# Optimization experiments

Measured on AMD Instinct MI355X. Metric: run time of the kernel, lower is better.

The kernel has to match this reference:

```python
import jax, jax.numpy as jnp
import numpy as np
from jax import lax

SIGMA = 0.03
ALPHA = 1.0
MASK_VALUE = -1e-8
SAMPLE_NUM = 131072  # static stand-in for the dynamic edge-pixel count


def _sobel_edges(images):
    # images: [n,3,h,w]; torch code uses only channel 0 when c==3
    kx = jnp.array([[-1., 0., 1.], [-2., 0., 2.], [-1., 0., 1.]], dtype=images.dtype).reshape(1, 1, 3, 3)
    ky = jnp.array([[1., 2., 1.], [0., 0., 0.], [-1., -2., -1.]], dtype=images.dtype).reshape(1, 1, 3, 3)
    x = images[:, :1]
    dn = ('NCHW', 'OIHW', 'NCHW')
    gx = lax.conv_general_dilated(x, kx, (1, 1), 'VALID', dimension_numbers=dn)
    gy = lax.conv_general_dilated(x, ky, (1, 1), 'VALID', dimension_numbers=dn)
    edges = jnp.sqrt(gx * gx + gy * gy)
    thetas = jnp.arctan2(gy, gx)
    pad = ((0, 0), (0, 0), (1, 1), (1, 1))
    return jnp.pad(edges, pad), jnp.pad(thetas, pad)


def _per_image_loss(inp, tgt, msk, edge, theta, ra, rd, rp, h, w):
    # all flat vectors of length P = h*w; ra:[S], rd:[4,S], rp:[2S]
    # --- edge-guided sampling ---
    emax = edge.max()
    emask = edge >= 0.1 * emax
    minlen = jnp.maximum(emask.sum(), 1)
    edge_idx = jnp.argsort(jnp.logical_not(emask), stable=True)  # edge pixels first
    anchor_pix = edge_idx[ra % minlen]
    theta_a = theta[anchor_pix]
    row_a = anchor_pix // w
    col_a = anchor_pix % w
    sign = jnp.array([-1., -1., 1., 1.], dtype=inp.dtype)[:, None]
    dist = (rd.astype(inp.dtype) + 2.0) * sign  # magnitudes in [2,31)
    col4 = jnp.clip(col_a[None, :] + jnp.round(dist * jnp.cos(theta_a)[None, :]).astype(jnp.int32), 0, w - 1)
    row4 = jnp.clip(row_a[None, :] + jnp.round(dist * jnp.sin(theta_a)[None, :]).astype(jnp.int32), 0, h - 1)
    pix = row4 * w + col4  # sub2ind, [4,S]
    A = jnp.concatenate([pix[0], pix[1], pix[2]])  # [3S]
    B = jnp.concatenate([pix[1], pix[2], pix[3]])
    # --- random sampling among valid (targets > threshold) pixels ---
    vmask = tgt > MASK_VALUE
    nvalid = jnp.maximum(vmask.sum(), 1)
    vidx = jnp.argsort(jnp.logical_not(vmask), stable=True)
    sh = rp % nvalid
    rA = vidx[sh[0::2]]
    rB = vidx[sh[1::2]]
    Ai = jnp.concatenate([A, rA])  # [4S]
    Bi = jnp.concatenate([B, rB])
    iA, iB = inp[Ai], inp[Bi]
    tA, tB = tgt[Ai], tgt[Bi]
    mA, mB = msk[Ai], msk[Bi]
    # --- ranking loss ---
    ratio = (tA + 1e-6) / (tB + 1e-6)
    hi = 1.0 + SIGMA
    lo = 1.0 / hi
    mask_eq = (ratio < hi) & (ratio > lo)
    labels = jnp.where(ratio >= hi, 1.0, 0.0) + jnp.where(ratio <= lo, -1.0, 0.0)
    cm = mA * mB
    equal_loss = (iA - iB) ** 2 * mask_eq.astype(inp.dtype) * cm
    unequal_loss = jnp.log1p(jnp.exp((iB - iA) * labels)) * (~mask_eq).astype(inp.dtype) * cm
    return ALPHA * equal_loss.mean() + unequal_loss.mean()


def reference(inputs, targets, images, rand_anchor, rand_dist, rand_perm):
    n, c, h, w = targets.shape
    masks = (targets > MASK_VALUE).astype(targets.dtype)
    edges, thetas = _sobel_edges(images)
    P = h * w
    flat = lambda x: x.reshape(n, P)
    per_img = lambda i, t, m, e, th, ra, rd, rp: _per_image_loss(i, t, m, e, th, ra, rd, rp, h, w)
    losses = jax.vmap(per_img)(flat(inputs), flat(targets), flat(masks), flat(edges), flat(thetas),
                               rand_anchor, rand_dist, rand_perm)
    return (losses.sum() / n).astype(jnp.float32)


def setup_inputs() -> dict:
    key = jax.random.key(0)
    k1, k2, k3, k4, k5, k6 = jax.random.split(key, 6)
    n, h, w = 4, 768, 1024
    P = h * w
    S = SAMPLE_NUM
    return {
        'inputs': jax.random.normal(k1, (n, 1, h, w), dtype=jnp.float32),
        'targets': jax.random.uniform(k2, (n, 1, h, w), dtype=jnp.float32),
        'images': jax.random.uniform(k3, (n, 3, h, w), dtype=jnp.float32),
        'rand_anchor': jax.random.randint(k4, (n, S), 0, P, dtype=jnp.int32),
        'rand_dist': jax.random.randint(k5, (n, 4, S), 0, 29, dtype=jnp.int32),
        'rand_perm': jax.random.randint(k6, (n, 2 * S), 0, P, dtype=jnp.int32),
    }
```

## Files before the change

kernel.cpp:

```cpp
#include <hip/hip_runtime.h>
#include <math.h>

#define W 1024
#define H 768
#define PIX (W*H)
#define NIMG 4
#define SNUM 131072
#define BPI 3072
#define NB (NIMG*BPI)
#define MASKV (-1e-8f)

__device__ __forceinline__ void sobel_g(const float* __restrict__ img, int y, int x,
                                        float& gx, float& gy) {
    const float* r0 = img + (y - 1) * W + x;
    const float* r1 = r0 + W;
    const float* r2 = r1 + W;
    float a00 = r0[-1], a01 = r0[0], a02 = r0[1];
    float a10 = r1[-1],              a12 = r1[1];
    float a20 = r2[-1], a21 = r2[0], a22 = r2[1];
    gx = (a02 - a00) + 2.f * (a12 - a10) + (a22 - a20);
    gy = (a00 - a20) + 2.f * (a01 - a21) + (a02 - a22);
}

__global__ void prep_kernel(const float* __restrict__ inputs,
                            const float* __restrict__ targets,
                            const float* __restrict__ images,
                            float2* __restrict__ pairIT,
                            unsigned long long* __restrict__ vBits,
                            float* __restrict__ blockmax,
                            int* __restrict__ blkV) {
    int b = blockIdx.x, t = threadIdx.x;
    int i = b / BPI, bLoc = b - i * BPI;
    int gp = bLoc * 256 + t;
    int y = gp >> 10, x = gp & (W - 1);
    const float* img = images + (size_t)i * 3 * PIX;
    float e = 0.f;
    if (y >= 1 && y <= H - 2 && x >= 1 && x <= W - 2) {
        float gx, gy;
        sobel_g(img, y, x, gx, gy);
        e = sqrtf(gx * gx + gy * gy);
    }
    size_t off = (size_t)i * PIX + gp;
    float inv = inputs[off], tgv = targets[off];
    pairIT[off] = make_float2(inv, tgv);
    unsigned long long m = __ballot(tgv > MASKV);
    __shared__ float sm[256];
    __shared__ int sc[4];
    if ((t & 63) == 0) { vBits[off >> 6] = m; sc[t >> 6] = __popcll(m); }
    sm[t] = e;
    __syncthreads();
    for (int o = 128; o > 0; o >>= 1) {
        if (t < o) sm[t] = fmaxf(sm[t], sm[t + o]);
        __syncthreads();
    }
    if (t == 0) { blockmax[b] = sm[0]; blkV[b] = sc[0] + sc[1] + sc[2] + sc[3]; }
}

__global__ void compact_kernel(const float* __restrict__ images,
                               const float* __restrict__ blockmax,
                               const int* __restrict__ blkV,
                               const unsigned long long* __restrict__ vBits,
                               float2* __restrict__ anchorSeg,
                               int* __restrict__ compVSeg,
                               int* __restrict__ cntE,
                               int* __restrict__ SVg,
                               int* __restrict__ vtotG) {
    int b = blockIdx.x, t = threadIdx.x;
    int i = b / BPI, bLoc = b - i * BPI;

    __shared__ float sf[256];
    const float* bm = blockmax + i * BPI;
    float mx = 0.f;
#pragma unroll
    for (int k = 0; k < 12; k++) mx = fmaxf(mx, bm[t + k * 256]);
    sf[t] = mx;
    __syncthreads();
    for (int o = 128; o > 0; o >>= 1) {
        if (t < o) sf[t] = fmaxf(sf[t], sf[t + o]);
        __syncthreads();
    }
    float thr = 0.1f * sf[0];

    int gp = bLoc * 256 + t;
    int y = gp >> 10, x = gp & (W - 1);
    const float* img = images + (size_t)i * 3 * PIX;
    float e = 0.f, gx = 0.f, gy = 0.f;
    bool inner = (y >= 1 && y <= H - 2 && x >= 1 && x <= W - 2);
    if (inner) { sobel_g(img, y, x, gx, gy); e = sqrtf(gx * gx + gy * gy); }
    bool isE = (e >= thr);

    int lane = t & 63, w = t >> 6;
    unsigned long long mE = __ballot(isE);
    size_t woff = ((size_t)i * PIX + bLoc * 256) >> 6;
    unsigned long long mV = vBits[woff + w];
    __shared__ int sW[4], sWV[4];
    if (lane == 0) { sW[w] = __popcll(mE); sWV[w] = __popcll(mV); }
    __syncthreads();
    int baseE = 0, baseV = 0;
    for (int k = 0; k < w; k++) { baseE += sW[k]; baseV += sWV[k]; }
    if (t == 0) cntE[b] = sW[0] + sW[1] + sW[2] + sW[3];
    unsigned long long lm = (1ull << lane) - 1ull;
    if (isE) {
        float th = inner ? atan2f(gy, gx) : 0.f;
        int rank = baseE + __popcll(mE & lm);
        anchorSeg[(size_t)i * PIX + bLoc * 256 + rank] = make_float2(__int_as_float(gp), th);
    }
    if ((mV >> lane) & 1) {
        int rank = baseV + __popcll(mV & lm);
        compVSeg[(size_t)i * PIX + bLoc * 256 + rank] = gp;
    }

    if (bLoc == 0) {
        __syncthreads();
        __shared__ int sT[256];
        const int* bv = blkV + i * BPI;
        int loc[12]; int tot = 0;
#pragma unroll
        for (int k = 0; k < 12; k++) { loc[k] = bv[t * 12 + k]; tot += loc[k]; }
        sT[t] = tot;
        __syncthreads();
        for (int o = 1; o < 256; o <<= 1) {
            int v = (t >= o) ? sT[t - o] : 0;
            __syncthreads();
            sT[t] += v;
            __syncthreads();
        }
        int run = sT[t] - tot;
        int* sv = SVg + i * BPI;
#pragma unroll
        for (int k = 0; k < 12; k++) { sv[t * 12 + k] = run; run += loc[k]; }
        if (t == 255) vtotG[i] = sT[255];
    }
}

__device__ __forceinline__ void pair_term(float2 a, float2 b, float& eqs, float& uns) {
    float cm = ((a.y > MASKV) ? 1.f : 0.f) * ((b.y > MASKV) ? 1.f : 0.f);
    float ratio = (a.y + 1e-6f) / (b.y + 1e-6f);
    const float HIv = 1.03f;
    const float LOv = (float)(1.0 / 1.03);
    bool eq = (ratio < HIv) && (ratio > LOv);
    if (eq) {
        float d = a.x - b.x;
        eqs += d * d * cm;
    } else {
        float label = ((ratio >= HIv) ? 1.f : 0.f) + ((ratio <= LOv) ? -1.f : 0.f);
        uns += log1pf(expf((b.x - a.x) * label)) * cm;
    }
}

__global__ void loss_kernel(const float2* __restrict__ pairIT,
                            const float2* __restrict__ anchorSeg,
                            const int* __restrict__ compVSeg,
                            const int* __restrict__ cntE,
                            const int* __restrict__ SVg,
                            const int* __restrict__ vtotG,
                            const int* __restrict__ ra, const int* __restrict__ rd,
                            const int* __restrict__ rp,
                            float2* __restrict__ partials) {
    int i = blockIdx.y, t = threadIdx.x;
    __shared__ int S[BPI];
    __shared__ int sT[256];
    {
        const int* ce = cntE + i * BPI;
        int loc[12]; int tot = 0;
#pragma unroll
        for (int k = 0; k < 12; k++) { loc[k] = ce[t * 12 + k]; tot += loc[k]; }
        sT[t] = tot;
        __syncthreads();
        for (int o = 1; o < 256; o <<= 1) {
            int v = (t >= o) ? sT[t - o] : 0;
            __syncthreads();
            sT[t] += v;
            __syncthreads();
        }
        int run = sT[t] - tot;
#pragma unroll
        for (int k = 0; k < 12; k++) { S[t * 12 + k] = run; run += loc[k]; }
        __syncthreads();
    }
    int eT = sT[255];
    int vT = vtotG[i];
    int nval = (vT > 0) ? vT : 1;

    int s = blockIdx.x * 256 + t;
    const float2* pIT = pairIT + (size_t)i * PIX;

    int j = ra[(size_t)i * SNUM + s] % eT;
    int lo = 0, hi = BPI - 1;
#pragma unroll
    for (int k = 0; k < 12; k++) {
        int mid = (lo + hi + 1) >> 1;
        if (S[mid] <= j) lo = mid; else hi = mid - 1;
    }
    float2 ac = anchorSeg[(size_t)i * PIX + lo * 256 + (j - S[lo])];
    int anchor = __float_as_int(ac.x);
    float sv = sinf(ac.y), cv = cosf(ac.y);
    int row_a = anchor >> 10, col_a = anchor & (W - 1);

    int pix4[4];
#pragma unroll
    for (int k = 0; k < 4; k++) {
        int r = rd[((size_t)i * 4 + k) * SNUM + s];
        float dist = ((float)r + 2.0f) * ((k < 2) ? -1.f : 1.f);
        int cc = col_a + (int)rintf(dist * cv);
        int rr = row_a + (int)rintf(dist * sv);
        cc = min(max(cc, 0), W - 1);
        rr = min(max(rr, 0), H - 1);
        pix4[k] = (rr << 10) | cc;
    }
    int2 rr2 = *(const int2*)(rp + (size_t)i * 2 * SNUM + 2 * s);
    int r0 = rr2.x % nval, r1 = rr2.y % nval;
    int A, B;
    if ((vT == PIX) || (vT == 0)) {
        A = r0; B = r1;
    } else {
        const int* SV = SVg + i * BPI;
        int lo2 = 0, hi2 = BPI - 1;
        int lo3 = 0, hi3 = BPI - 1;
#pragma unroll
        for (int k = 0; k < 12; k++) {
            int m2 = (lo2 + hi2 + 1) >> 1;
            if (SV[m2] <= r0) lo2 = m2; else hi2 = m2 - 1;
            int m3 = (lo3 + hi3 + 1) >> 1;
            if (SV[m3] <= r1) lo3 = m3; else hi3 = m3 - 1;
        }
        A = compVSeg[(size_t)i * PIX + lo2 * 256 + (r0 - SV[lo2])];
        B = compVSeg[(size_t)i * PIX + lo3 * 256 + (r1 - SV[lo3])];
    }

    float2 a0 = pIT[pix4[0]], a1 = pIT[pix4[1]], a2 = pIT[pix4[2]], a3 = pIT[pix4[3]];
    float2 b0 = pIT[A], b1 = pIT[B];
    float eqs = 0.f, uns = 0.f;
    pair_term(a0, a1, eqs, uns);
    pair_term(a1, a2, eqs, uns);
    pair_term(a2, a3, eqs, uns);
    pair_term(b0, b1, eqs, uns);

    __shared__ float sEq[256], sUn[256];
    sEq[t] = eqs; sUn[t] = uns;
    __syncthreads();
    for (int o = 128; o > 0; o >>= 1) {
        if (t < o) { sEq[t] += sEq[t + o]; sUn[t] += sUn[t + o]; }
        __syncthreads();
    }
    if (t == 0)
        partials[i * 512 + blockIdx.x] = make_float2(sEq[0], sUn[0]);
}

__global__ void final_kernel(const float2* __restrict__ partials, float* __restrict__ out) {
    int t = threadIdx.x;
    double acc = 0.0;
#pragma unroll
    for (int k = 0; k < 8; k++) {
        float2 p = partials[t + k * 256];
        acc += (double)p.x + (double)p.y;
    }
    __shared__ double sm[256];
    sm[t] = acc;
    __syncthreads();
    for (int o = 128; o > 0; o >>= 1) {
        if (t < o) sm[t] += sm[t + o];
        __syncthreads();
    }
    if (t == 0) {
        double denom = 4.0 * (double)SNUM;
        out[0] = (float)(sm[0] / denom / (double)NIMG);
    }
}

extern "C" void kernel_launch(void* const* d_in, const int* in_sizes, int n_in,
                              void* d_out, int out_size, void* d_ws, size_t ws_size,
                              hipStream_t stream) {
    const float* inputs  = (const float*)d_in[0];
    const float* targets = (const float*)d_in[1];
    const float* images  = (const float*)d_in[2];
    const int* ra = (const int*)d_in[3];
    const int* rd = (const int*)d_in[4];
    const int* rp = (const int*)d_in[5];
    float* out = (float*)d_out;

    char* ws = (char*)d_ws;
    int*      vtotG    = (int*)ws;
    float*    blockmax = (float*)(ws + 1024);
    int*      blkV     = (int*)(ws + 50176);
    int*      cntE     = (int*)(ws + 99328);
    int*      SVg      = (int*)(ws + 148480);
    float2*   partials = (float2*)(ws + 197632);
    unsigned long long* vBits = (unsigned long long*)(ws + 262144);
    float2*   pairIT   = (float2*)(ws + 1048576);
    float2*   anchorSeg= (float2*)(ws + 26214400);
    int*      compVSeg = (int*)(ws + 51380224);

    prep_kernel<<<NB, 256, 0, stream>>>(inputs, targets, images,
                                        pairIT, vBits, blockmax, blkV);
    compact_kernel<<<NB, 256, 0, stream>>>(images, blockmax, blkV, vBits,
                                           anchorSeg, compVSeg, cntE, SVg, vtotG);
    loss_kernel<<<dim3(512, NIMG), 256, 0, stream>>>(pairIT, anchorSeg, compVSeg,
                                                     cntE, SVg, vtotG,
                                                     ra, rd, rp, partials);
    final_kernel<<<1, 256, 0, stream>>>(partials, out);
}
```

Measured before the change: 187.1 us.

## Fuse prep and compaction into one cooperative kernel with shared-memory Sobel reuse

Merges the two preprocessing kernels into a single cooperative kernel of 1024 persistent blocks, each handling 12 units of 256 pixels. The Sobel magnitude and angle are kept in shared memory (24 KB) between phases, separated by a grid-wide sync, so the image stencil is not recomputed. Valid-pixel compaction moves into the first phase, which removes the vBits buffer. The cost is a grid sync, heavy shared-memory use under 4-blocks-per-CU launch bounds, and atan2 now computed for every pixel; if the cooperative launch fails, it falls back to two plain kernels.

```diff
diff --git a/kernel.cpp b/kernel.cpp
--- a/kernel.cpp
+++ b/kernel.cpp
@@ -1,5 +1,8 @@
 #include <hip/hip_runtime.h>
+#include <hip/hip_cooperative_groups.h>
 #include <math.h>
+
+namespace cg = cooperative_groups;
 
 #define W 1024
 #define H 768
@@ -7,7 +10,8 @@
 #define NIMG 4
 #define SNUM 131072
 #define BPI 3072
-#define NB (NIMG*BPI)
+#define UPB 12
+#define FPB 1024
 #define MASKV (-1e-8f)
 
 __device__ __forceinline__ void sobel_g(const float* __restrict__ img, int y, int x,
@@ -22,95 +26,110 @@
     gy = (a00 - a20) + 2.f * (a01 - a21) + (a02 - a22);
 }
 
-__global__ void prep_kernel(const float* __restrict__ inputs,
-                            const float* __restrict__ targets,
-                            const float* __restrict__ images,
-                            float2* __restrict__ pairIT,
-                            unsigned long long* __restrict__ vBits,
-                            float* __restrict__ blockmax,
-                            int* __restrict__ blkV) {
-    int b = blockIdx.x, t = threadIdx.x;
-    int i = b / BPI, bLoc = b - i * BPI;
-    int gp = bLoc * 256 + t;
-    int y = gp >> 10, x = gp & (W - 1);
+__device__ void phaseA(const float* __restrict__ inputs, const float* __restrict__ targets,
+                       const float* __restrict__ images,
+                       float2* __restrict__ pairIT, int* __restrict__ compVSeg,
+                       float* __restrict__ blockmax, int* __restrict__ blkV,
+                       float* sE, float* sTh)
+{
+    __shared__ float sRed[256];
+    __shared__ int sW[4];
+    int blk = blockIdx.x, t = threadIdx.x;
+    int i = blk >> 8, bb = blk & 255;
     const float* img = images + (size_t)i * 3 * PIX;
-    float e = 0.f;
-    if (y >= 1 && y <= H - 2 && x >= 1 && x <= W - 2) {
-        float gx, gy;
-        sobel_g(img, y, x, gx, gy);
-        e = sqrtf(gx * gx + gy * gy);
-    }
-    size_t off = (size_t)i * PIX + gp;
-    float inv = inputs[off], tgv = targets[off];
-    pairIT[off] = make_float2(inv, tgv);
-    unsigned long long m = __ballot(tgv > MASKV);
-    __shared__ float sm[256];
-    __shared__ int sc[4];
-    if ((t & 63) == 0) { vBits[off >> 6] = m; sc[t >> 6] = __popcll(m); }
-    sm[t] = e;
+    int lane = t & 63, w = t >> 6;
+    unsigned long long lm = (1ull << lane) - 1ull;
+
+    float bmax = 0.f;
+    for (int k = 0; k < UPB; k++) {
+        int unit = bb * UPB + k;
+        int gp = unit * 256 + t;
+        int y = gp >> 10, x = gp & (W - 1);
+        float e = 0.f, th = 0.f;
+        if (y >= 1 && y <= H - 2 && x >= 1 && x <= W - 2) {
+            float gx, gy;
+            sobel_g(img, y, x, gx, gy);
+            e = sqrtf(gx * gx + gy * gy);
+            th = atan2f(gy, gx);
+        }
+        if (sE) { sE[k * 256 + t] = e; sTh[k * 256 + t] = th; }
+        bmax = fmaxf(bmax, e);
+        size_t off = (size_t)i * PIX + gp;
+        float inv = inputs[off], tgv = targets[off];
+        pairIT[off] = make_float2(inv, tgv);
+        bool v = tgv > MASKV;
+        unsigned long long mV = __ballot(v);
+        __syncthreads();
+        if (lane == 0) sW[w] = __popcll(mV);
+        __syncthreads();
+        int base = 0;
+        for (int q = 0; q < w; q++) base += sW[q];
+        if (t == 0) blkV[i * BPI + unit] = sW[0] + sW[1] + sW[2] + sW[3];
+        if (v) compVSeg[(size_t)i * PIX + unit * 256 + base + __popcll(mV & lm)] = gp;
+    }
+    __syncthreads();
+    sRed[t] = bmax;
     __syncthreads();
     for (int o = 128; o > 0; o >>= 1) {
-        if (t < o) sm[t] = fmaxf(sm[t], sm[t + o]);
-        __syncthreads();
-    }
-    if (t == 0) { blockmax[b] = sm[0]; blkV[b] = sc[0] + sc[1] + sc[2] + sc[3]; }
-}
-
-__global__ void compact_kernel(const float* __restrict__ images,
-                               const float* __restrict__ blockmax,
-                               const int* __restrict__ blkV,
-                               const unsigned long long* __restrict__ vBits,
-                               float2* __restrict__ anchorSeg,
-                               int* __restrict__ compVSeg,
-                               int* __restrict__ cntE,
-                               int* __restrict__ SVg,
-                               int* __restrict__ vtotG) {
-    int b = blockIdx.x, t = threadIdx.x;
-    int i = b / BPI, bLoc = b - i * BPI;
-
-    __shared__ float sf[256];
-    const float* bm = blockmax + i * BPI;
-    float mx = 0.f;
-#pragma unroll
-    for (int k = 0; k < 12; k++) mx = fmaxf(mx, bm[t + k * 256]);
-    sf[t] = mx;
+        if (t < o) sRed[t] = fmaxf(sRed[t], sRed[t + o]);
+        __syncthreads();
+    }
+    if (t == 0) blockmax[blk] = sRed[0];
+}
+
+__device__ void phaseB(const float* __restrict__ images,
+                       const float* __restrict__ blockmax, const int* __restrict__ blkV,
+                       float2* __restrict__ anchorSeg, int* __restrict__ cntE,
+                       int* __restrict__ SVg, int* __restrict__ vtotG,
+                       const float* sE, const float* sTh)
+{
+    __shared__ float sRed2[256];
+    __shared__ int sW2[4];
+    int blk = blockIdx.x, t = threadIdx.x;
+    int i = blk >> 8, bb = blk & 255;
+    const float* img = images + (size_t)i * 3 * PIX;
+    int lane = t & 63, w = t >> 6;
+    unsigned long long lm = (1ull << lane) - 1ull;
+
+    const float* bm = blockmax + i * 256;
+    sRed2[t] = bm[t];
     __syncthreads();
     for (int o = 128; o > 0; o >>= 1) {
-        if (t < o) sf[t] = fmaxf(sf[t], sf[t + o]);
-        __syncthreads();
-    }
-    float thr = 0.1f * sf[0];
-
-    int gp = bLoc * 256 + t;
-    int y = gp >> 10, x = gp & (W - 1);
-    const float* img = images + (size_t)i * 3 * PIX;
-    float e = 0.f, gx = 0.f, gy = 0.f;
-    bool inner = (y >= 1 && y <= H - 2 && x >= 1 && x <= W - 2);
-    if (inner) { sobel_g(img, y, x, gx, gy); e = sqrtf(gx * gx + gy * gy); }
-    bool isE = (e >= thr);
-
-    int lane = t & 63, w = t >> 6;
-    unsigned long long mE = __ballot(isE);
-    size_t woff = ((size_t)i * PIX + bLoc * 256) >> 6;
-    unsigned long long mV = vBits[woff + w];
-    __shared__ int sW[4], sWV[4];
-    if (lane == 0) { sW[w] = __popcll(mE); sWV[w] = __popcll(mV); }
-    __syncthreads();
-    int baseE = 0, baseV = 0;
-    for (int k = 0; k < w; k++) { baseE += sW[k]; baseV += sWV[k]; }
-    if (t == 0) cntE[b] = sW[0] + sW[1] + sW[2] + sW[3];
-    unsigned long long lm = (1ull << lane) - 1ull;
-    if (isE) {
-        float th = inner ? atan2f(gy, gx) : 0.f;
-        int rank = baseE + __popcll(mE & lm);
-        anchorSeg[(size_t)i * PIX + bLoc * 256 + rank] = make_float2(__int_as_float(gp), th);
-    }
-    if ((mV >> lane) & 1) {
-        int rank = baseV + __popcll(mV & lm);
-        compVSeg[(size_t)i * PIX + bLoc * 256 + rank] = gp;
-    }
-
-    if (bLoc == 0) {
+        if (t < o) sRed2[t] = fmaxf(sRed2[t], sRed2[t + o]);
+        __syncthreads();
+    }
+    float thr = 0.1f * sRed2[0];
+
+    for (int k = 0; k < UPB; k++) {
+        int unit = bb * UPB + k;
+        int gp = unit * 256 + t;
+        float e, th;
+        if (sE) {
+            e = sE[k * 256 + t]; th = sTh[k * 256 + t];
+        } else {
+            int y = gp >> 10, x = gp & (W - 1);
+            e = 0.f; th = 0.f;
+            if (y >= 1 && y <= H - 2 && x >= 1 && x <= W - 2) {
+                float gx, gy;
+                sobel_g(img, y, x, gx, gy);
+                e = sqrtf(gx * gx + gy * gy);
+                th = atan2f(gy, gx);
+            }
+        }
+        bool isE = (e >= thr);
+        unsigned long long mE = __ballot(isE);
+        __syncthreads();
+        if (lane == 0) sW2[w] = __popcll(mE);
+        __syncthreads();
+        int base = 0;
+        for (int q = 0; q < w; q++) base += sW2[q];
+        if (t == 0) cntE[i * BPI + unit] = sW2[0] + sW2[1] + sW2[2] + sW2[3];
+        if (isE)
+            anchorSeg[(size_t)i * PIX + unit * 256 + base + __popcll(mE & lm)] =
+                make_float2(__int_as_float(gp), th);
+    }
+
+    if (bb == 0) {
         __syncthreads();
         __shared__ int sT[256];
         const int* bv = blkV + i * BPI;
@@ -131,6 +150,36 @@
         for (int k = 0; k < 12; k++) { sv[t * 12 + k] = run; run += loc[k]; }
         if (t == 255) vtotG[i] = sT[255];
     }
+}
+
+__global__ __launch_bounds__(256, 4) void fused_prep(
+    const float* __restrict__ inputs, const float* __restrict__ targets,
+    const float* __restrict__ images,
+    float2* __restrict__ pairIT,
+    float* __restrict__ blockmax, int* __restrict__ blkV, int* __restrict__ cntE,
+    float2* __restrict__ anchorSeg, int* __restrict__ compVSeg,
+    int* __restrict__ SVg, int* __restrict__ vtotG)
+{
+    cg::grid_group grid = cg::this_grid();
+    __shared__ float sE[UPB * 256];
+    __shared__ float sTh[UPB * 256];
+    phaseA(inputs, targets, images, pairIT, compVSeg, blockmax, blkV, sE, sTh);
+    grid.sync();
+    phaseB(images, blockmax, blkV, anchorSeg, cntE, SVg, vtotG, sE, sTh);
+}
+
+__global__ void prepA_kernel(const float* __restrict__ inputs,
+                             const float* __restrict__ targets,
+                             const float* __restrict__ images,
+                             float2* __restrict__ pairIT, int* __restrict__ compVSeg,
+                             float* __restrict__ blockmax, int* __restrict__ blkV) {
+    phaseA(inputs, targets, images, pairIT, compVSeg, blockmax, blkV, nullptr, nullptr);
+}
+__global__ void prepB_kernel(const float* __restrict__ images,
+                             const float* __restrict__ blockmax, const int* __restrict__ blkV,
+                             float2* __restrict__ anchorSeg, int* __restrict__ cntE,
+                             int* __restrict__ SVg, int* __restrict__ vtotG) {
+    phaseB(images, blockmax, blkV, anchorSeg, cntE, SVg, vtotG, nullptr, nullptr);
 }
 
 __device__ __forceinline__ void pair_term(float2 a, float2 b, float& eqs, float& uns) {
@@ -282,19 +331,26 @@
     char* ws = (char*)d_ws;
     int*      vtotG    = (int*)ws;
     float*    blockmax = (float*)(ws + 1024);
-    int*      blkV     = (int*)(ws + 50176);
-    int*      cntE     = (int*)(ws + 99328);
-    int*      SVg      = (int*)(ws + 148480);
-    float2*   partials = (float2*)(ws + 197632);
-    unsigned long long* vBits = (unsigned long long*)(ws + 262144);
+    int*      blkV     = (int*)(ws + 16384);
+    int*      cntE     = (int*)(ws + 65536);
+    int*      SVg      = (int*)(ws + 114688);
+    float2*   partials = (float2*)(ws + 163840);
     float2*   pairIT   = (float2*)(ws + 1048576);
     float2*   anchorSeg= (float2*)(ws + 26214400);
     int*      compVSeg = (int*)(ws + 51380224);
 
-    prep_kernel<<<NB, 256, 0, stream>>>(inputs, targets, images,
-                                        pairIT, vBits, blockmax, blkV);
-    compact_kernel<<<NB, 256, 0, stream>>>(images, blockmax, blkV, vBits,
-                                           anchorSeg, compVSeg, cntE, SVg, vtotG);
+    void* args[] = {(void*)&inputs, (void*)&targets, (void*)&images,
+                    (void*)&pairIT, (void*)&blockmax, (void*)&blkV, (void*)&cntE,
+                    (void*)&anchorSeg, (void*)&compVSeg, (void*)&SVg, (void*)&vtotG};
+    hipError_t cerr = hipLaunchCooperativeKernel(reinterpret_cast<void*>(fused_prep),
+                                                 dim3(FPB), dim3(256), args, 0, stream);
+    if (cerr != hipSuccess) {
+        (void)hipGetLastError();
+        prepA_kernel<<<FPB, 256, 0, stream>>>(inputs, targets, images,
+                                              pairIT, compVSeg, blockmax, blkV);
+        prepB_kernel<<<FPB, 256, 0, stream>>>(images, blockmax, blkV,
+                                              anchorSeg, cntE, SVg, vtotG);
+    }
     loss_kernel<<<dim3(512, NIMG), 256, 0, stream>>>(pairIT, anchorSeg, compVSeg,
                                                      cntE, SVg, vtotG,
                                                      ra, rd, rp, partials);
```

Result: slower. 324.4 us (+73.3%).

## Move valid-pixel compaction into prep kernel and coarsen compact kernel blocks

Applied to the files above, without the earlier changes.

The valid-mask compaction is now done directly in the prep kernel, so the vBits buffer no longer has to be written and read back. The compact kernel now launches 1024 blocks, each handling 12 units of 256 pixels. This spreads the redundant per-block global-max reduction over 12 times fewer blocks. The trade-off is a serial loop with extra syncthreads per unit and less parallelism in the compact kernel.

```diff
diff --git a/kernel.cpp b/kernel.cpp
--- a/kernel.cpp
+++ b/kernel.cpp
@@ -7,7 +7,9 @@
 #define NIMG 4
 #define SNUM 131072
 #define BPI 3072
-#define NB (NIMG*BPI)
+#define NBP (NIMG*BPI)
+#define UPB 12
+#define NBC 1024
 #define MASKV (-1e-8f)
 
 __device__ __forceinline__ void sobel_g(const float* __restrict__ img, int y, int x,
@@ -26,12 +28,12 @@
                             const float* __restrict__ targets,
                             const float* __restrict__ images,
                             float2* __restrict__ pairIT,
-                            unsigned long long* __restrict__ vBits,
+                            int* __restrict__ compVSeg,
                             float* __restrict__ blockmax,
                             int* __restrict__ blkV) {
     int b = blockIdx.x, t = threadIdx.x;
-    int i = b / BPI, bLoc = b - i * BPI;
-    int gp = bLoc * 256 + t;
+    int i = b / BPI, unit = b - i * BPI;
+    int gp = unit * 256 + t;
     int y = gp >> 10, x = gp & (W - 1);
     const float* img = images + (size_t)i * 3 * PIX;
     float e = 0.f;
@@ -43,74 +45,76 @@
     size_t off = (size_t)i * PIX + gp;
     float inv = inputs[off], tgv = targets[off];
     pairIT[off] = make_float2(inv, tgv);
-    unsigned long long m = __ballot(tgv > MASKV);
+
+    int lane = t & 63, w = t >> 6;
+    bool v = tgv > MASKV;
+    unsigned long long mV = __ballot(v);
     __shared__ float sm[256];
-    __shared__ int sc[4];
-    if ((t & 63) == 0) { vBits[off >> 6] = m; sc[t >> 6] = __popcll(m); }
+    __shared__ int sW[4];
+    if (lane == 0) sW[w] = __popcll(mV);
     sm[t] = e;
     __syncthreads();
+    int base = 0;
+    for (int q = 0; q < w; q++) base += sW[q];
+    if (t == 0) blkV[b] = sW[0] + sW[1] + sW[2] + sW[3];
+    if (v) compVSeg[off - t + base + __popcll(mV & ((1ull << lane) - 1ull))] = gp;
     for (int o = 128; o > 0; o >>= 1) {
         if (t < o) sm[t] = fmaxf(sm[t], sm[t + o]);
         __syncthreads();
     }
-    if (t == 0) { blockmax[b] = sm[0]; blkV[b] = sc[0] + sc[1] + sc[2] + sc[3]; }
+    if (t == 0) blockmax[b] = sm[0];
 }
 
 __global__ void compact_kernel(const float* __restrict__ images,
                                const float* __restrict__ blockmax,
                                const int* __restrict__ blkV,
-                               const unsigned long long* __restrict__ vBits,
                                float2* __restrict__ anchorSeg,
-                               int* __restrict__ compVSeg,
                                int* __restrict__ cntE,
                                int* __restrict__ SVg,
                                int* __restrict__ vtotG) {
-    int b = blockIdx.x, t = threadIdx.x;
-    int i = b / BPI, bLoc = b - i * BPI;
-
-    __shared__ float sf[256];
+    int blk = blockIdx.x, t = threadIdx.x;
+    int i = blk >> 8, bb = blk & 255;
+    const float* img = images + (size_t)i * 3 * PIX;
+    int lane = t & 63, w = t >> 6;
+    unsigned long long lm = (1ull << lane) - 1ull;
+
+    __shared__ float sRed[256];
+    __shared__ int sW2[4];
     const float* bm = blockmax + i * BPI;
     float mx = 0.f;
 #pragma unroll
     for (int k = 0; k < 12; k++) mx = fmaxf(mx, bm[t + k * 256]);
-    sf[t] = mx;
+    sRed[t] = mx;
     __syncthreads();
     for (int o = 128; o > 0; o >>= 1) {
-        if (t < o) sf[t] = fmaxf(sf[t], sf[t + o]);
-        __syncthreads();
-    }
-    float thr = 0.1f * sf[0];
-
-    int gp = bLoc * 256 + t;
-    int y = gp >> 10, x = gp & (W - 1);
-    const float* img = images + (size_t)i * 3 * PIX;
-    float e = 0.f, gx = 0.f, gy = 0.f;
-    bool inner = (y >= 1 && y <= H - 2 && x >= 1 && x <= W - 2);
-    if (inner) { sobel_g(img, y, x, gx, gy); e = sqrtf(gx * gx + gy * gy); }
-    bool isE = (e >= thr);
-
-    int lane = t & 63, w = t >> 6;
-    unsigned long long mE = __ballot(isE);
-    size_t woff = ((size_t)i * PIX + bLoc * 256) >> 6;
-    unsigned long long mV = vBits[woff + w];
-    __shared__ int sW[4], sWV[4];
-    if (lane == 0) { sW[w] = __popcll(mE); sWV[w] = __popcll(mV); }
-    __syncthreads();
-    int baseE = 0, baseV = 0;
-    for (int k = 0; k < w; k++) { baseE += sW[k]; baseV += sWV[k]; }
-    if (t == 0) cntE[b] = sW[0] + sW[1] + sW[2] + sW[3];
-    unsigned long long lm = (1ull << lane) - 1ull;
-    if (isE) {
-        float th = inner ? atan2f(gy, gx) : 0.f;
-        int rank = baseE + __popcll(mE & lm);
-        anchorSeg[(size_t)i * PIX + bLoc * 256 + rank] = make_float2(__int_as_float(gp), th);
-    }
-    if ((mV >> lane) & 1) {
-        int rank = baseV + __popcll(mV & lm);
-        compVSeg[(size_t)i * PIX + bLoc * 256 + rank] = gp;
-    }
-
-    if (bLoc == 0) {
+        if (t < o) sRed[t] = fmaxf(sRed[t], sRed[t + o]);
+        __syncthreads();
+    }
+    float thr = 0.1f * sRed[0];
+
+    for (int k = 0; k < UPB; k++) {
+        int unit = bb * UPB + k;
+        int gp = unit * 256 + t;
+        int y = gp >> 10, x = gp & (W - 1);
+        float e = 0.f, gx = 0.f, gy = 0.f;
+        bool inner = (y >= 1 && y <= H - 2 && x >= 1 && x <= W - 2);
+        if (inner) { sobel_g(img, y, x, gx, gy); e = sqrtf(gx * gx + gy * gy); }
+        bool isE = (e >= thr);
+        unsigned long long mE = __ballot(isE);
+        __syncthreads();
+        if (lane == 0) sW2[w] = __popcll(mE);
+        __syncthreads();
+        int base = 0;
+        for (int q = 0; q < w; q++) base += sW2[q];
+        if (t == 0) cntE[i * BPI + unit] = sW2[0] + sW2[1] + sW2[2] + sW2[3];
+        if (isE) {
+            float th = inner ? atan2f(gy, gx) : 0.f;
+            anchorSeg[(size_t)i * PIX + unit * 256 + base + __popcll(mE & lm)] =
+                make_float2(__int_as_float(gp), th);
+        }
+    }
+
+    if (bb == 0) {
         __syncthreads();
         __shared__ int sT[256];
         const int* bv = blkV + i * BPI;
@@ -286,15 +290,14 @@
     int*      cntE     = (int*)(ws + 99328);
     int*      SVg      = (int*)(ws + 148480);
     float2*   partials = (float2*)(ws + 197632);
-    unsigned long long* vBits = (unsigned long long*)(ws + 262144);
     float2*   pairIT   = (float2*)(ws + 1048576);
     float2*   anchorSeg= (float2*)(ws + 26214400);
     int*      compVSeg = (int*)(ws + 51380224);
 
-    prep_kernel<<<NB, 256, 0, stream>>>(inputs, targets, images,
-                                        pairIT, vBits, blockmax, blkV);
-    compact_kernel<<<NB, 256, 0, stream>>>(images, blockmax, blkV, vBits,
-                                           anchorSeg, compVSeg, cntE, SVg, vtotG);
+    prep_kernel<<<NBP, 256, 0, stream>>>(inputs, targets, images,
+                                         pairIT, compVSeg, blockmax, blkV);
+    compact_kernel<<<NBC, 256, 0, stream>>>(images, blockmax, blkV,
+                                            anchorSeg, cntE, SVg, vtotG);
     loss_kernel<<<dim3(512, NIMG), 256, 0, stream>>>(pairIT, anchorSeg, compVSeg,
                                                      cntE, SVg, vtotG,
                                                      ra, rd, rp, partials);
```

New measurement: 180.1 us. 1.04x faster.
